# Optimization experiments

Measured on AMD Instinct MI355X. Metric: run time of the kernel, lower is better.

Reference implementation:

```python
import jax, jax.numpy as jnp
import numpy as np
import math

NUM_HEADS = 32
NUM_KV_HEADS = 8
HEAD_DIM = 64
ROPE_THETA = 150000.0


def rotate_half(x):
    half = x.shape[-1] // 2
    return jnp.concatenate([-x[..., half:], x[..., :half]], axis=-1)


def setup_inputs() -> dict:
    key = jax.random.key(0)
    k1, k2, k3, k4, k5 = jax.random.split(key, 5)
    B, S, H = 2, 2048, 2048
    qkv_size = (NUM_HEADS + 2 * NUM_KV_HEADS) * HEAD_DIM  # 3072
    scale = 1.0 / math.sqrt(H)
    return {
        "hidden_states": jax.random.normal(k1, (B, S, H), jnp.float32),
        "position_ids": jnp.arange(S, dtype=jnp.int64 if jax.config.jax_enable_x64 else jnp.int32)[None, :],
        "qkv_w": jax.random.normal(k2, (qkv_size, H), jnp.float32) * scale,
        "qkv_b": jax.random.normal(k3, (qkv_size,), jnp.float32) * 0.01,
        "o_w": jax.random.normal(k4, (H, NUM_HEADS * HEAD_DIM), jnp.float32) * scale,
        "o_b": jax.random.normal(k5, (H,), jnp.float32) * 0.01,
    }


def reference(hidden_states, position_ids, qkv_w, qkv_b, o_w, o_b):
    B, S, _ = hidden_states.shape
    g = NUM_HEADS // NUM_KV_HEADS  # query heads per kv head
    d = HEAD_DIM

    qkv = hidden_states @ qkv_w.T + qkv_b  # [B,S,(H+2KV)*d]
    qkv = qkv.reshape(B, S, NUM_KV_HEADS, g + 2, d)
    q = qkv[:, :, :, :g, :].reshape(B, S, NUM_HEADS, d).transpose(0, 2, 1, 3)   # [B,Hq,S,d]
    k = qkv[:, :, :, g, :].transpose(0, 2, 1, 3)                                 # [B,Hkv,S,d]
    v = qkv[:, :, :, g + 1, :].transpose(0, 2, 1, 3)                             # [B,Hkv,S,d]

    # HF-style RoPE: cos/sin [S, d]
    inv_freq = 1.0 / (ROPE_THETA ** (jnp.arange(0, d, 2, dtype=jnp.float32) / d))
    freqs = jnp.outer(position_ids.reshape(-1).astype(jnp.float32), inv_freq)    # [S, d/2]
    emb = jnp.concatenate([freqs, freqs], axis=-1)                               # [S, d]
    cos = jnp.cos(emb)[None, None]                                               # [1,1,S,d]
    sin = jnp.sin(emb)[None, None]
    q = q * cos + rotate_half(q) * sin
    k = k * cos + rotate_half(k) * sin

    # GQA: repeat_interleave kv heads to match query heads
    k = jnp.repeat(k, g, axis=1)  # [B,Hq,S,d]
    v = jnp.repeat(v, g, axis=1)

    scores = jnp.einsum("bhqd,bhkd->bhqk", q, k) / math.sqrt(d)  # [B,Hq,S,S]
    attn = jax.nn.softmax(scores, axis=-1)
    out = jnp.einsum("bhqk,bhkd->bhqd", attn, v)
    out = out.transpose(0, 2, 1, 3).reshape(B, S, NUM_HEADS * d)
    return out @ o_w.T + o_b
```

## Files before the change

### kernel.cpp

```cpp
#include <hip/hip_runtime.h>
#include <math.h>

#define NHQ 32
#define NKV 8
#define HD 64
#define QKV_DIM 3072
#define MODEL_DIM 2048
#define QSCALE 0.1803368801111204f

typedef __attribute__((ext_vector_type(4))) float     f32x4;
typedef __attribute__((ext_vector_type(8))) _Float16  half8;
typedef __attribute__((ext_vector_type(4))) _Float16  half4v;
typedef __attribute__((ext_vector_type(2))) __fp16    fp16x2;

#define ASYNC_COPY16(g, l)                                                        \
    __builtin_amdgcn_global_load_lds(                                             \
        (const __attribute__((address_space(1))) void*)(g),                       \
        (__attribute__((address_space(3))) void*)(l), 16, 0, 0)

__device__ __forceinline__ float fast_exp2(float x)
{
#if __has_builtin(__builtin_amdgcn_exp2f)
    return __builtin_amdgcn_exp2f(x);
#else
    float r;
    asm volatile("v_exp_f32 %0, %1\ns_nop 0" : "=v"(r) : "v"(x));
    return r;
#endif
}

__global__ __launch_bounds__(256)
void f32_to_f16_kernel(const float* __restrict__ src, _Float16* __restrict__ dst, int n4)
{
    int i = blockIdx.x * 256 + threadIdx.x;
    if (i < n4) {
        float4 v = ((const float4*)src)[i];
        half4v h = { (_Float16)v.x, (_Float16)v.y, (_Float16)v.z, (_Float16)v.w };
        ((half4v*)dst)[i] = h;
    }
}

__global__ __launch_bounds__(256)
void sincos_table_kernel(const int* __restrict__ pos, float* __restrict__ tab, int S)
{
    int i = blockIdx.x * 256 + threadIdx.x;
    if (i < S * 32) {
        int s = i >> 5, fi = i & 31;
        float p = (float)pos[s];
        float inv_freq = powf(150000.0f, -(float)fi * (1.0f / 32.0f));
        float ang = p * inv_freq;
        tab[s * 64 + fi]      = cosf(ang);
        tab[s * 64 + 32 + fi] = sinf(ang);
    }
}

template<int MODE>
__global__ __launch_bounds__(256, 3)
void gemm_f16_mfma(const _Float16* __restrict__ A, const _Float16* __restrict__ W,
                   const float* __restrict__ bias, void* __restrict__ Cout,
                   const float* __restrict__ tab, int M, int N, int K, int S)
{
    __shared__ _Float16 As[3][128 * 32];
    __shared__ _Float16 Bs[3][128 * 32];

    const int t    = threadIdx.x;
    const int w    = t >> 6;
    const int lane = t & 63;
    const int quad = lane >> 4, l15 = lane & 15;
    const size_t m0 = (size_t)blockIdx.y * 128;
    const size_t n0 = (size_t)blockIdx.x * 128;
    const int wm = (w >> 1) * 64, wn = (w & 1) * 64;

    const int sr   = t >> 2;
    const int klog = ((t & 3) ^ ((sr >> 1) & 3)) * 8;
    const _Float16* ag0 = A + (m0 + sr) * K + klog;
    const _Float16* ag1 = A + (m0 + 64 + sr) * K + klog;
    const _Float16* bg0 = W + (n0 + sr) * K + klog;
    const _Float16* bg1 = W + (n0 + 64 + sr) * K + klog;

    const int xk8 = (quad ^ ((l15 >> 1) & 3)) * 8;

    f32x4 acc[4][4];
#pragma unroll
    for (int i = 0; i < 4; i++)
#pragma unroll
        for (int j = 0; j < 4; j++) acc[i][j] = (f32x4){0.f, 0.f, 0.f, 0.f};

    const int nt = K >> 5;

#define STAGE_TILE(bi, kt_)                                         \
    do {                                                            \
        const int _k0 = (kt_) * 32;                                 \
        ASYNC_COPY16(ag0 + _k0, &As[bi][w * 512]);                  \
        ASYNC_COPY16(ag1 + _k0, &As[bi][2048 + w * 512]);           \
        ASYNC_COPY16(bg0 + _k0, &Bs[bi][w * 512]);                  \
        ASYNC_COPY16(bg1 + _k0, &Bs[bi][2048 + w * 512]);           \
    } while (0)

    STAGE_TILE(0, 0);
    STAGE_TILE(1, 1);
    asm volatile("s_waitcnt vmcnt(4)" ::: "memory");
    __builtin_amdgcn_s_barrier();
    __builtin_amdgcn_sched_barrier(0);

    int bc = 0;
    for (int kt = 0; kt < nt; ++kt) {
        const _Float16* Ab = &As[bc][0];
        const _Float16* Bb = &Bs[bc][0];

        half8 af[4], bf[4];
#pragma unroll
        for (int i = 0; i < 4; i++) {
            af[i] = *(const half8*)(Ab + (wm + i * 16 + l15) * 32 + xk8);
            bf[i] = *(const half8*)(Bb + (wn + i * 16 + l15) * 32 + xk8);
        }

        if (kt + 2 < nt) {
            int bs = bc + 2; if (bs >= 3) bs -= 3;
            STAGE_TILE(bs, kt + 2);
        }

        __builtin_amdgcn_s_setprio(1);
#pragma unroll
        for (int i = 0; i < 4; i++)
#pragma unroll
            for (int j = 0; j < 4; j++)
                acc[i][j] = __builtin_amdgcn_mfma_f32_16x16x32_f16(af[i], bf[j], acc[i][j], 0, 0, 0);
        __builtin_amdgcn_s_setprio(0);

        if (kt + 1 < nt) {
            if (kt + 2 < nt) asm volatile("s_waitcnt vmcnt(4)" ::: "memory");
            else             asm volatile("s_waitcnt vmcnt(0)" ::: "memory");
            __builtin_amdgcn_s_barrier();
            __builtin_amdgcn_sched_barrier(0);
        }
        bc = bc + 1; if (bc == 3) bc = 0;
    }
#undef STAGE_TILE

    float bv[4];
#pragma unroll
    for (int j = 0; j < 4; j++) bv[j] = bias[n0 + wn + j * 16 + l15];

    const int ct = (int)(((n0 + wn) >> 6) % 6);

#pragma unroll
    for (int i = 0; i < 4; i++)
#pragma unroll
        for (int r = 0; r < 4; r++) {
            const size_t row = m0 + wm + i * 16 + quad * 4 + r;
            float v[4];
#pragma unroll
            for (int j = 0; j < 4; j++) v[j] = acc[i][j][r] + bv[j];

            if (MODE == 2 && ct != 5) {
                const float* tc = tab + (size_t)(row % S) * 64;
                const float ca = tc[l15],      sa = tc[32 + l15];
                const float cb = tc[16 + l15], sb = tc[48 + l15];
                const float qs = (ct < 4) ? QSCALE : 1.0f;
                const float n0v = v[0] * ca - v[2] * sa;
                const float n1v = v[1] * cb - v[3] * sb;
                const float n2v = v[2] * ca + v[0] * sa;
                const float n3v = v[3] * cb + v[1] * sb;
                v[0] = n0v * qs; v[1] = n1v * qs; v[2] = n2v * qs; v[3] = n3v * qs;
            }

            const size_t col = n0 + wn + l15;
#pragma unroll
            for (int j = 0; j < 4; j++) {
                if (MODE != 0) ((_Float16*)Cout)[row * N + col + j * 16] = (_Float16)v[j];
                else           ((float*)Cout)[row * N + col + j * 16] = v[j];
            }
        }
}

__global__ __launch_bounds__(256)
void transpose_v_kernel(const _Float16* __restrict__ qkv, _Float16* __restrict__ vtg, int BS)
{
    __shared__ _Float16 tile[64 * 72];
    const int t = threadIdx.x;
    const int tb = blockIdx.x * 64;
    const int g = blockIdx.y;
    const int voff = (g * 6 + 5) * 64;

    const int tok = t >> 2, dsub = (t & 3) * 16;
    const _Float16* src = qkv + (size_t)(tb + tok) * QKV_DIM + voff + dsub;
    *(half8*)&tile[tok * 72 + dsub]     = *(const half8*)(src);
    *(half8*)&tile[tok * 72 + dsub + 8] = *(const half8*)(src + 8);
    __syncthreads();

    const int d = t >> 2, tsub = (t & 3) * 16;
    half8 a, c;
#pragma unroll
    for (int i = 0; i < 8; i++) a[i] = tile[(tsub + i) * 72 + d];
#pragma unroll
    for (int i = 0; i < 8; i++) c[i] = tile[(tsub + 8 + i) * 72 + d];
    _Float16* dst = vtg + ((size_t)g * 64 + d) * BS + tb + tsub;
    *(half8*)dst       = a;
    *(half8*)(dst + 8) = c;
}

__global__ __launch_bounds__(256)
void attn_mfma(const _Float16* __restrict__ qkv, const _Float16* __restrict__ vtg,
               _Float16* __restrict__ out, int B, int S)
{
    __shared__ _Float16 Ks[64 * 72];
    __shared__ _Float16 VsT[80 * 72];
    __shared__ _Float16 Ps[4][32 * 72];

    const int t = threadIdx.x, w = t >> 6, lane = t & 63;
    const int quad = lane >> 4, l15 = lane & 15;
    const int b = blockIdx.z, g = blockIdx.y;
    const int q0 = blockIdx.x * 32;
    const int qoff = (g * 6 + w) * 64;
    const int koff = (g * 6 + 4) * 64;

    half8 qf[2][2];
#pragma unroll
    for (int s = 0; s < 2; s++) {
        const _Float16* qp = qkv + (size_t)(b * S + q0 + s * 16 + l15) * QKV_DIM + qoff;
        qf[s][0] = *(const half8*)(qp + quad * 8);
        qf[s][1] = *(const half8*)(qp + 32 + quad * 8);
    }

    for (int idx = 64 * 72 + t; idx < 80 * 72; idx += 256)
        VsT[idx] = (idx < 65 * 72) ? (_Float16)1.0f : (_Float16)0.0f;

    f32x4 O[2][4], L[2];
#pragma unroll
    for (int s = 0; s < 2; s++) {
        L[s] = (f32x4){0.f, 0.f, 0.f, 0.f};
#pragma unroll
        for (int dt = 0; dt < 4; dt++) O[s][dt] = (f32x4){0.f, 0.f, 0.f, 0.f};
    }

    const int kst_tok = t >> 2;
    const int kst_d   = (t & 3) * 16;
    const int vst_d   = t >> 3;
    const int vst_sub = (t & 7) * 8;

    const _Float16* kbase  = qkv + (size_t)(b * S + kst_tok) * QKV_DIM + koff + kst_d;
    const _Float16* vbase0 = vtg + ((size_t)g * 64 + vst_d) * (size_t)(B * S) + b * S + vst_sub;
    const _Float16* vbase1 = vtg + ((size_t)g * 64 + 32 + vst_d) * (size_t)(B * S) + b * S + vst_sub;

    half8 kr0 = *(const half8*)(kbase);
    half8 kr1 = *(const half8*)(kbase + 8);
    half8 vr0 = *(const half8*)(vbase0);
    half8 vr1 = *(const half8*)(vbase1);

    for (int kt = 0; kt < S; kt += 64) {
        *(half8*)&Ks[kst_tok * 72 + kst_d]      = kr0;
        *(half8*)&Ks[kst_tok * 72 + kst_d + 8]  = kr1;
        *(half8*)&VsT[vst_d * 72 + vst_sub]        = vr0;
        *(half8*)&VsT[(32 + vst_d) * 72 + vst_sub] = vr1;
        __syncthreads();

        if (kt + 64 < S) {
            kr0 = *(const half8*)(kbase + (size_t)(kt + 64) * QKV_DIM);
            kr1 = *(const half8*)(kbase + (size_t)(kt + 64) * QKV_DIM + 8);
            vr0 = *(const half8*)(vbase0 + kt + 64);
            vr1 = *(const half8*)(vbase1 + kt + 64);
        }

        half8 kf[4][2];
#pragma unroll
        for (int mt = 0; mt < 4; mt++) {
            kf[mt][0] = *(const half8*)&Ks[(mt * 16 + l15) * 72 + quad * 8];
            kf[mt][1] = *(const half8*)&Ks[(mt * 16 + l15) * 72 + 32 + quad * 8];
        }
        f32x4 sacc[2][4];
#pragma unroll
        for (int s = 0; s < 2; s++)
#pragma unroll
            for (int mt = 0; mt < 4; mt++) {
                f32x4 z = (f32x4){0.f, 0.f, 0.f, 0.f};
                z = __builtin_amdgcn_mfma_f32_16x16x32_f16(kf[mt][0], qf[s][0], z, 0, 0, 0);
                z = __builtin_amdgcn_mfma_f32_16x16x32_f16(kf[mt][1], qf[s][1], z, 0, 0, 0);
                sacc[s][mt] = z;
            }

#pragma unroll
        for (int s = 0; s < 2; s++)
#pragma unroll
            for (int mt = 0; mt < 4; mt++) {
                fp16x2 pa = __builtin_amdgcn_cvt_pkrtz(fast_exp2(sacc[s][mt][0]),
                                                       fast_exp2(sacc[s][mt][1]));
                fp16x2 pb = __builtin_amdgcn_cvt_pkrtz(fast_exp2(sacc[s][mt][2]),
                                                       fast_exp2(sacc[s][mt][3]));
                uint2 u;
                u.x = __builtin_bit_cast(unsigned int, pa);
                u.y = __builtin_bit_cast(unsigned int, pb);
                *(uint2*)&Ps[w][(s * 16 + l15) * 72 + mt * 16 + quad * 4] = u;
            }
        asm volatile("s_waitcnt lgkmcnt(0)" ::: "memory");

        half8 pf[2][2];
#pragma unroll
        for (int s = 0; s < 2; s++) {
            pf[s][0] = *(const half8*)&Ps[w][(s * 16 + l15) * 72 + quad * 8];
            pf[s][1] = *(const half8*)&Ps[w][(s * 16 + l15) * 72 + 32 + quad * 8];
        }
#pragma unroll
        for (int dt = 0; dt < 4; dt++) {
            half8 vv0 = *(const half8*)&VsT[(dt * 16 + l15) * 72 + quad * 8];
            half8 vv1 = *(const half8*)&VsT[(dt * 16 + l15) * 72 + 32 + quad * 8];
#pragma unroll
            for (int s = 0; s < 2; s++) {
                O[s][dt] = __builtin_amdgcn_mfma_f32_16x16x32_f16(pf[s][0], vv0, O[s][dt], 0, 0, 0);
                O[s][dt] = __builtin_amdgcn_mfma_f32_16x16x32_f16(pf[s][1], vv1, O[s][dt], 0, 0, 0);
            }
        }
        {
            half8 lv0 = *(const half8*)&VsT[(64 + l15) * 72 + quad * 8];
            half8 lv1 = *(const half8*)&VsT[(64 + l15) * 72 + 32 + quad * 8];
#pragma unroll
            for (int s = 0; s < 2; s++) {
                L[s] = __builtin_amdgcn_mfma_f32_16x16x32_f16(pf[s][0], lv0, L[s], 0, 0, 0);
                L[s] = __builtin_amdgcn_mfma_f32_16x16x32_f16(pf[s][1], lv1, L[s], 0, 0, 0);
            }
        }
        __syncthreads();
    }

    const int hq = g * 4 + w;
#pragma unroll
    for (int s = 0; s < 2; s++)
#pragma unroll
        for (int r = 0; r < 4; r++) {
            const float lr = __shfl(L[s][r], lane & 48, 64);
            const float ir = 1.0f / lr;
            const size_t row = (size_t)(b * S + q0 + s * 16 + quad * 4 + r);
#pragma unroll
            for (int dt = 0; dt < 4; dt++)
                out[row * (NHQ * HD) + hq * 64 + dt * 16 + l15] = (_Float16)(O[s][dt][r] * ir);
        }
}

extern "C" void kernel_launch(void* const* d_in, const int* in_sizes, int n_in,
                              void* d_out, int out_size, void* d_ws, size_t ws_size,
                              hipStream_t stream)
{
    const float* hidden = (const float*)d_in[0];
    const int*   pos    = (const int*)d_in[1];
    const float* qkv_w  = (const float*)d_in[2];
    const float* qkv_b  = (const float*)d_in[3];
    const float* o_w    = (const float*)d_in[4];
    const float* o_b    = (const float*)d_in[5];
    float* out = (float*)d_out;

    const int S  = in_sizes[1];
    const int BS = in_sizes[0] / MODEL_DIM;
    const int B  = BS / S;

    _Float16* hA   = (_Float16*)d_ws;
    _Float16* hW1  = hA   + (size_t)BS * MODEL_DIM;
    _Float16* hW2  = hW1  + (size_t)QKV_DIM * MODEL_DIM;
    _Float16* qkvh = hW2  + (size_t)MODEL_DIM * MODEL_DIM;
    _Float16* atth = qkvh + (size_t)BS * QKV_DIM;
    float*    tab  = (float*)(atth + (size_t)BS * MODEL_DIM);
    _Float16* vtg  = (_Float16*)(tab + (size_t)S * 64);

    f32_to_f16_kernel<<<(BS * MODEL_DIM / 4 + 255) / 256, 256, 0, stream>>>(hidden, hA, BS * MODEL_DIM / 4);
    f32_to_f16_kernel<<<(QKV_DIM * MODEL_DIM / 4 + 255) / 256, 256, 0, stream>>>(qkv_w, hW1, QKV_DIM * MODEL_DIM / 4);
    f32_to_f16_kernel<<<(MODEL_DIM * MODEL_DIM / 4 + 255) / 256, 256, 0, stream>>>(o_w, hW2, MODEL_DIM * MODEL_DIM / 4);
    sincos_table_kernel<<<(S * 32 + 255) / 256, 256, 0, stream>>>(pos, tab, S);

    gemm_f16_mfma<2><<<dim3(QKV_DIM / 128, BS / 128), 256, 0, stream>>>(
        hA, hW1, qkv_b, qkvh, tab, BS, QKV_DIM, MODEL_DIM, S);

    transpose_v_kernel<<<dim3(BS / 64, NKV), 256, 0, stream>>>(qkvh, vtg, BS);

    attn_mfma<<<dim3(S / 32, NKV, B), 256, 0, stream>>>(qkvh, vtg, atth, B, S);

    gemm_f16_mfma<0><<<dim3(MODEL_DIM / 128, BS / 128), 256, 0, stream>>>(
        atth, hW2, o_b, out, nullptr, BS, MODEL_DIM, MODEL_DIM, S);
}
```

Measured before the change: 331.4 us.

## Keep softmax probabilities in registers via permlane swaps and use 128-key tiles

Removes the per-wave LDS round trip for the probability matrix. The exp'd scores are rearranged across lanes with v_permlane32/16_swap so they can feed the PV MFMA directly as the A operand. The row-sum ones-vector now lives in a register instead of an extra LDS row. The KV tile grows from 64 to 128 keys per sync, halving barriers per key, and launch bounds request 4 blocks per CU. This raises per-thread register use for the larger staging buffers, and it relies on the permlane lane mapping matching the MFMA operand layout.

```diff
diff --git a/kernel.cpp b/kernel.cpp
--- a/kernel.cpp
+++ b/kernel.cpp
@@ -12,6 +12,7 @@
 typedef __attribute__((ext_vector_type(8))) _Float16  half8;
 typedef __attribute__((ext_vector_type(4))) _Float16  half4v;
 typedef __attribute__((ext_vector_type(2))) __fp16    fp16x2;
+typedef __attribute__((ext_vector_type(4))) unsigned  uint32x4;
 
 #define ASYNC_COPY16(g, l)                                                        \
     __builtin_amdgcn_global_load_lds(                                             \
@@ -200,13 +201,14 @@
     *(half8*)(dst + 8) = c;
 }
 
-__global__ __launch_bounds__(256)
+#define KVB 128
+
+__global__ __launch_bounds__(256, 4)
 void attn_mfma(const _Float16* __restrict__ qkv, const _Float16* __restrict__ vtg,
                _Float16* __restrict__ out, int B, int S)
 {
-    __shared__ _Float16 Ks[64 * 72];
-    __shared__ _Float16 VsT[80 * 72];
-    __shared__ _Float16 Ps[4][32 * 72];
+    __shared__ _Float16 Ks[KVB * 72];
+    __shared__ _Float16 VsT[64 * 136];
 
     const int t = threadIdx.x, w = t >> 6, lane = t & 63;
     const int quad = lane >> 4, l15 = lane & 15;
@@ -223,8 +225,12 @@
         qf[s][1] = *(const half8*)(qp + 32 + quad * 8);
     }
 
-    for (int idx = 64 * 72 + t; idx < 80 * 72; idx += 256)
-        VsT[idx] = (idx < 65 * 72) ? (_Float16)1.0f : (_Float16)0.0f;
+    half8 lv;
+    {
+        const _Float16 one = (l15 == 0) ? (_Float16)1.0f : (_Float16)0.0f;
+#pragma unroll
+        for (int j = 0; j < 8; j++) lv[j] = one;
+    }
 
     f32x4 O[2][4], L[2];
 #pragma unroll
@@ -234,89 +240,108 @@
         for (int dt = 0; dt < 4; dt++) O[s][dt] = (f32x4){0.f, 0.f, 0.f, 0.f};
     }
 
-    const int kst_tok = t >> 2;
-    const int kst_d   = (t & 3) * 16;
+    const int kst_tok = t >> 1;
+    const int kst_d   = (t & 1) * 32;
     const int vst_d   = t >> 3;
-    const int vst_sub = (t & 7) * 8;
+    const int vst_sub = (t & 7) * 16;
 
     const _Float16* kbase  = qkv + (size_t)(b * S + kst_tok) * QKV_DIM + koff + kst_d;
     const _Float16* vbase0 = vtg + ((size_t)g * 64 + vst_d) * (size_t)(B * S) + b * S + vst_sub;
     const _Float16* vbase1 = vtg + ((size_t)g * 64 + 32 + vst_d) * (size_t)(B * S) + b * S + vst_sub;
 
-    half8 kr0 = *(const half8*)(kbase);
-    half8 kr1 = *(const half8*)(kbase + 8);
-    half8 vr0 = *(const half8*)(vbase0);
-    half8 vr1 = *(const half8*)(vbase1);
-
-    for (int kt = 0; kt < S; kt += 64) {
-        *(half8*)&Ks[kst_tok * 72 + kst_d]      = kr0;
-        *(half8*)&Ks[kst_tok * 72 + kst_d + 8]  = kr1;
-        *(half8*)&VsT[vst_d * 72 + vst_sub]        = vr0;
-        *(half8*)&VsT[(32 + vst_d) * 72 + vst_sub] = vr1;
+    half8 kr[4], vr[4];
+#pragma unroll
+    for (int i = 0; i < 4; i++) kr[i] = *(const half8*)(kbase + i * 8);
+    vr[0] = *(const half8*)(vbase0);
+    vr[1] = *(const half8*)(vbase0 + 8);
+    vr[2] = *(const half8*)(vbase1);
+    vr[3] = *(const half8*)(vbase1 + 8);
+
+    for (int kt = 0; kt < S; kt += KVB) {
+#pragma unroll
+        for (int i = 0; i < 4; i++)
+            *(half8*)&Ks[kst_tok * 72 + kst_d + i * 8] = kr[i];
+        *(half8*)&VsT[vst_d * 136 + vst_sub]            = vr[0];
+        *(half8*)&VsT[vst_d * 136 + vst_sub + 8]        = vr[1];
+        *(half8*)&VsT[(32 + vst_d) * 136 + vst_sub]     = vr[2];
+        *(half8*)&VsT[(32 + vst_d) * 136 + vst_sub + 8] = vr[3];
         __syncthreads();
 
-        if (kt + 64 < S) {
-            kr0 = *(const half8*)(kbase + (size_t)(kt + 64) * QKV_DIM);
-            kr1 = *(const half8*)(kbase + (size_t)(kt + 64) * QKV_DIM + 8);
-            vr0 = *(const half8*)(vbase0 + kt + 64);
-            vr1 = *(const half8*)(vbase1 + kt + 64);
-        }
-
-        half8 kf[4][2];
-#pragma unroll
-        for (int mt = 0; mt < 4; mt++) {
-            kf[mt][0] = *(const half8*)&Ks[(mt * 16 + l15) * 72 + quad * 8];
-            kf[mt][1] = *(const half8*)&Ks[(mt * 16 + l15) * 72 + 32 + quad * 8];
-        }
-        f32x4 sacc[2][4];
-#pragma unroll
-        for (int s = 0; s < 2; s++)
+        if (kt + KVB < S) {
+#pragma unroll
+            for (int i = 0; i < 4; i++)
+                kr[i] = *(const half8*)(kbase + (size_t)(kt + KVB) * QKV_DIM + i * 8);
+            vr[0] = *(const half8*)(vbase0 + kt + KVB);
+            vr[1] = *(const half8*)(vbase0 + kt + KVB + 8);
+            vr[2] = *(const half8*)(vbase1 + kt + KVB);
+            vr[3] = *(const half8*)(vbase1 + kt + KVB + 8);
+        }
+
+#pragma unroll
+        for (int hb = 0; hb < 2; hb++) {
+            const int kb = hb * 64;
+
+            half8 kf[4][2];
 #pragma unroll
             for (int mt = 0; mt < 4; mt++) {
-                f32x4 z = (f32x4){0.f, 0.f, 0.f, 0.f};
-                z = __builtin_amdgcn_mfma_f32_16x16x32_f16(kf[mt][0], qf[s][0], z, 0, 0, 0);
-                z = __builtin_amdgcn_mfma_f32_16x16x32_f16(kf[mt][1], qf[s][1], z, 0, 0, 0);
-                sacc[s][mt] = z;
+                kf[mt][0] = *(const half8*)&Ks[(kb + mt * 16 + l15) * 72 + quad * 8];
+                kf[mt][1] = *(const half8*)&Ks[(kb + mt * 16 + l15) * 72 + 32 + quad * 8];
             }
-
-#pragma unroll
-        for (int s = 0; s < 2; s++)
-#pragma unroll
-            for (int mt = 0; mt < 4; mt++) {
-                fp16x2 pa = __builtin_amdgcn_cvt_pkrtz(fast_exp2(sacc[s][mt][0]),
-                                                       fast_exp2(sacc[s][mt][1]));
-                fp16x2 pb = __builtin_amdgcn_cvt_pkrtz(fast_exp2(sacc[s][mt][2]),
-                                                       fast_exp2(sacc[s][mt][3]));
-                uint2 u;
-                u.x = __builtin_bit_cast(unsigned int, pa);
-                u.y = __builtin_bit_cast(unsigned int, pb);
-                *(uint2*)&Ps[w][(s * 16 + l15) * 72 + mt * 16 + quad * 4] = u;
+            f32x4 sacc[2][4];
+#pragma unroll
+            for (int s = 0; s < 2; s++)
+#pragma unroll
+                for (int mt = 0; mt < 4; mt++) {
+                    f32x4 z = (f32x4){0.f, 0.f, 0.f, 0.f};
+                    z = __builtin_amdgcn_mfma_f32_16x16x32_f16(kf[mt][0], qf[s][0], z, 0, 0, 0);
+                    z = __builtin_amdgcn_mfma_f32_16x16x32_f16(kf[mt][1], qf[s][1], z, 0, 0, 0);
+                    sacc[s][mt] = z;
+                }
+
+            unsigned u[2][4][2];
+#pragma unroll
+            for (int s = 0; s < 2; s++)
+#pragma unroll
+                for (int mt = 0; mt < 4; mt++) {
+                    fp16x2 pa = __builtin_amdgcn_cvt_pkrtz(fast_exp2(sacc[s][mt][0]),
+                                                           fast_exp2(sacc[s][mt][1]));
+                    fp16x2 pb = __builtin_amdgcn_cvt_pkrtz(fast_exp2(sacc[s][mt][2]),
+                                                           fast_exp2(sacc[s][mt][3]));
+                    u[s][mt][0] = __builtin_bit_cast(unsigned, pa);
+                    u[s][mt][1] = __builtin_bit_cast(unsigned, pb);
+                }
+
+            half8 pf[2][2];
+#pragma unroll
+            for (int s = 0; s < 2; s++)
+#pragma unroll
+                for (int h = 0; h < 2; h++) {
+                    uint32x4 pw;
+#pragma unroll
+                    for (int c = 0; c < 2; c++) {
+                        unsigned x = u[s][h * 2][c], y = u[s][h * 2 + 1][c];
+                        asm("v_permlane32_swap_b32 %0, %1" : "+v"(x), "+v"(y));
+                        asm("v_permlane16_swap_b32 %0, %1" : "+v"(x), "+v"(y));
+                        pw[c]     = x;
+                        pw[2 + c] = y;
+                    }
+                    pf[s][h] = __builtin_bit_cast(half8, pw);
+                }
+
+#pragma unroll
+            for (int dt = 0; dt < 4; dt++) {
+                half8 vv0 = *(const half8*)&VsT[(dt * 16 + l15) * 136 + kb + quad * 8];
+                half8 vv1 = *(const half8*)&VsT[(dt * 16 + l15) * 136 + kb + 32 + quad * 8];
+#pragma unroll
+                for (int s = 0; s < 2; s++) {
+                    O[s][dt] = __builtin_amdgcn_mfma_f32_16x16x32_f16(pf[s][0], vv0, O[s][dt], 0, 0, 0);
+                    O[s][dt] = __builtin_amdgcn_mfma_f32_16x16x32_f16(pf[s][1], vv1, O[s][dt], 0, 0, 0);
+                }
             }
-        asm volatile("s_waitcnt lgkmcnt(0)" ::: "memory");
-
-        half8 pf[2][2];
-#pragma unroll
-        for (int s = 0; s < 2; s++) {
-            pf[s][0] = *(const half8*)&Ps[w][(s * 16 + l15) * 72 + quad * 8];
-            pf[s][1] = *(const half8*)&Ps[w][(s * 16 + l15) * 72 + 32 + quad * 8];
-        }
-#pragma unroll
-        for (int dt = 0; dt < 4; dt++) {
-            half8 vv0 = *(const half8*)&VsT[(dt * 16 + l15) * 72 + quad * 8];
-            half8 vv1 = *(const half8*)&VsT[(dt * 16 + l15) * 72 + 32 + quad * 8];
 #pragma unroll
             for (int s = 0; s < 2; s++) {
-                O[s][dt] = __builtin_amdgcn_mfma_f32_16x16x32_f16(pf[s][0], vv0, O[s][dt], 0, 0, 0);
-                O[s][dt] = __builtin_amdgcn_mfma_f32_16x16x32_f16(pf[s][1], vv1, O[s][dt], 0, 0, 0);
-            }
-        }
-        {
-            half8 lv0 = *(const half8*)&VsT[(64 + l15) * 72 + quad * 8];
-            half8 lv1 = *(const half8*)&VsT[(64 + l15) * 72 + 32 + quad * 8];
-#pragma unroll
-            for (int s = 0; s < 2; s++) {
-                L[s] = __builtin_amdgcn_mfma_f32_16x16x32_f16(pf[s][0], lv0, L[s], 0, 0, 0);
-                L[s] = __builtin_amdgcn_mfma_f32_16x16x32_f16(pf[s][1], lv1, L[s], 0, 0, 0);
+                L[s] = __builtin_amdgcn_mfma_f32_16x16x32_f16(pf[s][0], lv, L[s], 0, 0, 0);
+                L[s] = __builtin_amdgcn_mfma_f32_16x16x32_f16(pf[s][1], lv, L[s], 0, 0, 0);
             }
         }
         __syncthreads();
```

Result: slower. 433.7 us (+30.9%).

## Relayout softmax probabilities in registers via permlane swaps instead of LDS

Applied to the files above, without the earlier changes.

The P matrix produced by the QK MFMA is converted from the accumulator layout to the A-operand layout with v_permlane32_swap/v_permlane16_swap cross-lane moves, so the per-wave Ps shared-memory round trip and its wait are gone. The ones row used to compute the row-sum L is now built as a register constant, so it is no longer kept in VsT. Both changes cut LDS traffic and LDS footprint, which may allow higher occupancy. The risk is a wrong permutation mapping, which would silently corrupt results, plus extra VALU permlane instructions.

```diff
diff --git a/kernel.cpp b/kernel.cpp
--- a/kernel.cpp
+++ b/kernel.cpp
@@ -12,6 +12,7 @@
 typedef __attribute__((ext_vector_type(8))) _Float16  half8;
 typedef __attribute__((ext_vector_type(4))) _Float16  half4v;
 typedef __attribute__((ext_vector_type(2))) __fp16    fp16x2;
+typedef __attribute__((ext_vector_type(4))) unsigned  uint32x4;
 
 #define ASYNC_COPY16(g, l)                                                        \
     __builtin_amdgcn_global_load_lds(                                             \
@@ -205,8 +206,7 @@
                _Float16* __restrict__ out, int B, int S)
 {
     __shared__ _Float16 Ks[64 * 72];
-    __shared__ _Float16 VsT[80 * 72];
-    __shared__ _Float16 Ps[4][32 * 72];
+    __shared__ _Float16 VsT[64 * 72];
 
     const int t = threadIdx.x, w = t >> 6, lane = t & 63;
     const int quad = lane >> 4, l15 = lane & 15;
@@ -223,8 +223,12 @@
         qf[s][1] = *(const half8*)(qp + 32 + quad * 8);
     }
 
-    for (int idx = 64 * 72 + t; idx < 80 * 72; idx += 256)
-        VsT[idx] = (idx < 65 * 72) ? (_Float16)1.0f : (_Float16)0.0f;
+    half8 lv;
+    {
+        const _Float16 one = (l15 == 0) ? (_Float16)1.0f : (_Float16)0.0f;
+#pragma unroll
+        for (int j = 0; j < 8; j++) lv[j] = one;
+    }
 
     f32x4 O[2][4], L[2];
 #pragma unroll
@@ -249,8 +253,8 @@
     half8 vr1 = *(const half8*)(vbase1);
 
     for (int kt = 0; kt < S; kt += 64) {
-        *(half8*)&Ks[kst_tok * 72 + kst_d]      = kr0;
-        *(half8*)&Ks[kst_tok * 72 + kst_d + 8]  = kr1;
+        *(half8*)&Ks[kst_tok * 72 + kst_d]         = kr0;
+        *(half8*)&Ks[kst_tok * 72 + kst_d + 8]     = kr1;
         *(half8*)&VsT[vst_d * 72 + vst_sub]        = vr0;
         *(half8*)&VsT[(32 + vst_d) * 72 + vst_sub] = vr1;
         __syncthreads();
@@ -268,38 +272,45 @@
             kf[mt][0] = *(const half8*)&Ks[(mt * 16 + l15) * 72 + quad * 8];
             kf[mt][1] = *(const half8*)&Ks[(mt * 16 + l15) * 72 + 32 + quad * 8];
         }
-        f32x4 sacc[2][4];
-#pragma unroll
-        for (int s = 0; s < 2; s++)
+
+        half8 pf[2][2];
+#pragma unroll
+        for (int s = 0; s < 2; s++) {
+            f32x4 sacc[4];
 #pragma unroll
             for (int mt = 0; mt < 4; mt++) {
                 f32x4 z = (f32x4){0.f, 0.f, 0.f, 0.f};
                 z = __builtin_amdgcn_mfma_f32_16x16x32_f16(kf[mt][0], qf[s][0], z, 0, 0, 0);
                 z = __builtin_amdgcn_mfma_f32_16x16x32_f16(kf[mt][1], qf[s][1], z, 0, 0, 0);
-                sacc[s][mt] = z;
-            }
-
-#pragma unroll
-        for (int s = 0; s < 2; s++)
+                sacc[mt] = z;
+            }
+
+            unsigned u[4][2];
 #pragma unroll
             for (int mt = 0; mt < 4; mt++) {
-                fp16x2 pa = __builtin_amdgcn_cvt_pkrtz(fast_exp2(sacc[s][mt][0]),
-                                                       fast_exp2(sacc[s][mt][1]));
-                fp16x2 pb = __builtin_amdgcn_cvt_pkrtz(fast_exp2(sacc[s][mt][2]),
-                                                       fast_exp2(sacc[s][mt][3]));
-                uint2 u;
-                u.x = __builtin_bit_cast(unsigned int, pa);
-                u.y = __builtin_bit_cast(unsigned int, pb);
-                *(uint2*)&Ps[w][(s * 16 + l15) * 72 + mt * 16 + quad * 4] = u;
-            }
-        asm volatile("s_waitcnt lgkmcnt(0)" ::: "memory");
-
-        half8 pf[2][2];
-#pragma unroll
-        for (int s = 0; s < 2; s++) {
-            pf[s][0] = *(const half8*)&Ps[w][(s * 16 + l15) * 72 + quad * 8];
-            pf[s][1] = *(const half8*)&Ps[w][(s * 16 + l15) * 72 + 32 + quad * 8];
-        }
+                fp16x2 pa = __builtin_amdgcn_cvt_pkrtz(fast_exp2(sacc[mt][0]),
+                                                       fast_exp2(sacc[mt][1]));
+                fp16x2 pb = __builtin_amdgcn_cvt_pkrtz(fast_exp2(sacc[mt][2]),
+                                                       fast_exp2(sacc[mt][3]));
+                u[mt][0] = __builtin_bit_cast(unsigned, pa);
+                u[mt][1] = __builtin_bit_cast(unsigned, pb);
+            }
+
+#pragma unroll
+            for (int h = 0; h < 2; h++) {
+                uint32x4 pw;
+#pragma unroll
+                for (int c = 0; c < 2; c++) {
+                    unsigned x = u[h * 2][c], y = u[h * 2 + 1][c];
+                    asm("v_permlane32_swap_b32 %0, %1" : "+v"(x), "+v"(y));
+                    asm("v_permlane16_swap_b32 %0, %1" : "+v"(x), "+v"(y));
+                    pw[c]     = x;
+                    pw[2 + c] = y;
+                }
+                pf[s][h] = __builtin_bit_cast(half8, pw);
+            }
+        }
+
 #pragma unroll
         for (int dt = 0; dt < 4; dt++) {
             half8 vv0 = *(const half8*)&VsT[(dt * 16 + l15) * 72 + quad * 8];
@@ -310,14 +321,10 @@
                 O[s][dt] = __builtin_amdgcn_mfma_f32_16x16x32_f16(pf[s][1], vv1, O[s][dt], 0, 0, 0);
             }
         }
-        {
-            half8 lv0 = *(const half8*)&VsT[(64 + l15) * 72 + quad * 8];
-            half8 lv1 = *(const half8*)&VsT[(64 + l15) * 72 + 32 + quad * 8];
-#pragma unroll
-            for (int s = 0; s < 2; s++) {
-                L[s] = __builtin_amdgcn_mfma_f32_16x16x32_f16(pf[s][0], lv0, L[s], 0, 0, 0);
-                L[s] = __builtin_amdgcn_mfma_f32_16x16x32_f16(pf[s][1], lv1, L[s], 0, 0, 0);
-            }
+#pragma unroll
+        for (int s = 0; s < 2; s++) {
+            L[s] = __builtin_amdgcn_mfma_f32_16x16x32_f16(pf[s][0], lv, L[s], 0, 0, 0);
+            L[s] = __builtin_amdgcn_mfma_f32_16x16x32_f16(pf[s][1], lv, L[s], 0, 0, 0);
         }
         __syncthreads();
     }
```

Result: faster. 314.9 us (-5.0%).
